# Kernel optimization log

Hardware: AMD Instinct MI355X
Metric: run time of the kernel (lower is better)

The kernel has to match this reference:

```python
import jax, jax.numpy as jnp
import numpy as np

B, C, T = 8, 512, 1024
EXP = 2
E = EXP * C          # 1024, gate/value width
H, HD = 8, 64        # heads, qk head dim
QK = H * HD          # 512
AVG_LEN = 512
EPS = 1e-5


def setup_inputs() -> dict:
    key = jax.random.key(0)
    ks = jax.random.split(key, 10)
    s = 0.02
    return {
        "x": jax.random.normal(ks[0], (B, C, T), jnp.float32),
        "W_in": jax.random.normal(ks[1], (2 * E, C), jnp.float32) * s,
        "b_in": jnp.zeros((2 * E,), jnp.float32),
        "W_attn": jax.random.normal(ks[2], (QK, C), jnp.float32) * s,
        "b_attn": jnp.zeros((QK,), jnp.float32),
        "w_q": 1.0 + jax.random.normal(ks[3], (QK,), jnp.float32) * 0.1,
        "b_q": jax.random.normal(ks[4], (QK,), jnp.float32) * 0.1,
        "w_k": 1.0 + jax.random.normal(ks[5], (QK,), jnp.float32) * 0.1,
        "b_k": jax.random.normal(ks[6], (QK,), jnp.float32) * 0.1,
        "W_out": jax.random.normal(ks[7], (C, E), jnp.float32) * s,
        "b_out": jnp.zeros((C,), jnp.float32),
        "gamma": jnp.ones((C,), jnp.float32),
    }


def reference(x, W_in, b_in, W_attn, b_attn, w_q, b_q, w_k, b_k, W_out, b_out, gamma):
    residual = x
    # mlp_in (1x1 conv) + SiLU, then chunk into gate u and value v, each (B,E,T)
    uv = jax.nn.silu(jnp.einsum('oc,bct->bot', W_in, x) + b_in[:, None])
    u, v = uv[:, :E], uv[:, E:]
    # mlp_attn (1x1 conv); no activation (activation_attn unused in forward)
    z = jnp.einsum('oc,bct->bot', W_attn, x) + b_attn[:, None]  # (B,QK,T)
    # depthwise 1x1 conv on cat(z,z) = two independent per-channel affines
    q = z * w_q[:, None] + b_q[:, None]
    k = z * w_k[:, None] + b_k[:, None]
    # split heads: q,k -> (B,H,T,HD); v -> (B,H,T,E//H)
    q = q.reshape(B, H, HD, T).transpose(0, 1, 3, 2)
    k = k.reshape(B, H, HD, T).transpose(0, 1, 3, 2)
    vh = v.reshape(B, H, E // H, T).transpose(0, 1, 3, 2)
    # entropy-invariant scale: (log n / log avg_len) / sqrt(d)
    scale = (np.log(T) / np.log(AVG_LEN)) / np.sqrt(HD)
    scores = jnp.einsum('bhqd,bhkd->bhqk', q, k) * jnp.float32(scale)
    attn = jax.nn.softmax(scores, axis=-1)
    o = jnp.einsum('bhqk,bhke->bhqe', attn, vh)        # (B,H,T,E//H)
    o = o.transpose(0, 1, 3, 2).reshape(B, E, T)       # back to (B,E,T)
    # gate, project out, residual + RMSNorm over channel dim
    out = jnp.einsum('ce,bet->bct', W_out, u * o) + b_out[:, None]
    y = residual + out
    rms = jax.lax.rsqrt(jnp.mean(y * y, axis=1, keepdims=True) + EPS)
    return y * rms * gamma[:, None]
```

## Files before the change

kernel.cpp:

```cpp
#include <hip/hip_runtime.h>

typedef __attribute__((ext_vector_type(8))) short short8;
typedef __attribute__((ext_vector_type(4))) float f32x4;
typedef __attribute__((ext_vector_type(16))) float f32x16;

__device__ __forceinline__ unsigned short f2b(float f) {
  union { float f; unsigned u; } x; x.f = f;
  unsigned r = (x.u + 0x7fffu + ((x.u >> 16) & 1u)) >> 16;
  return (unsigned short)r;
}
__device__ __forceinline__ float b2f(unsigned short b) {
  union { unsigned u; float f; } x; x.u = ((unsigned)b) << 16;
  return x.f;
}
__device__ __forceinline__ unsigned cvtpk(float lo, float hi) {
  unsigned r;
  asm("v_cvt_pk_bf16_f32 %0, %1, %2" : "=v"(r) : "v"(lo), "v"(hi));
  return r;
}
__device__ __forceinline__ void plswap(unsigned& a, unsigned& b) {
  asm volatile("v_permlane32_swap_b32 %0, %1" : "+v"(a), "+v"(b));
}

#define GLDS16(gp, lp)                                                                  \
  __builtin_amdgcn_global_load_lds((const __attribute__((address_space(1))) void*)(gp), \
                                   (__attribute__((address_space(3))) void*)(lp), 16, 0, 0)

__global__ void prep_w_kernel(const float* __restrict__ W_in, const float* __restrict__ W_attn,
                              const float* __restrict__ W_out, unsigned short* __restrict__ Wcat,
                              unsigned short* __restrict__ WoutB) {
  const int n1 = 2048 * 512, n2 = 512 * 512, n3 = 512 * 1024;
  for (int i = blockIdx.x * 256 + threadIdx.x; i < n1 + n2 + n3; i += gridDim.x * 256) {
    if (i < n1) Wcat[i] = f2b(W_in[i]);
    else if (i < n1 + n2) Wcat[i] = f2b(W_attn[i - n1]);
    else WoutB[i - n1 - n2] = f2b(W_out[i - n1 - n2]);
  }
}

__global__ __launch_bounds__(256) void transpose_x_kernel(const float* __restrict__ x,
                                                          unsigned short* __restrict__ xT) {
  __shared__ float tile[32][33];
  const int bid = blockIdx.x;
  const int b = bid & 7;
  const int rem = bid >> 3;
  const int c0 = (rem >> 5) << 5;
  const int t0 = (rem & 31) << 5;
  const int tj = threadIdx.x & 31, ti = threadIdx.x >> 5;
#pragma unroll
  for (int r = 0; r < 32; r += 8)
    tile[ti + r][tj] = x[(((size_t)b << 9) + c0 + ti + r) * 1024 + t0 + tj];
  __syncthreads();
#pragma unroll
  for (int r = 0; r < 32; r += 8)
    xT[(((size_t)b << 10) + t0 + ti + r) * 512 + c0 + tj] = f2b(tile[tj][ti + r]);
}

__device__ __forceinline__ void gemm_stage(const unsigned short* Ag, const unsigned short* Bg,
                                           int lda, int ldb, int k0, unsigned short* lsA,
                                           unsigned short* lsB, int buf, int sr, int sk,
                                           int ldst) {
  const int bb = buf * 8192;
  GLDS16(Ag + (size_t)sr * lda + k0 + sk, (char*)lsA + bb + ldst);
  GLDS16(Ag + (size_t)(sr + 64) * lda + k0 + sk, (char*)lsA + bb + 4096 + ldst);
  GLDS16(Bg + (size_t)sr * ldb + k0 + sk, (char*)lsB + bb + ldst);
  GLDS16(Bg + (size_t)(sr + 64) * ldb + k0 + sk, (char*)lsB + bb + 4096 + ldst);
}

__device__ __forceinline__ void gemm_bt_core(const unsigned short* __restrict__ Ag,
                                             const unsigned short* __restrict__ Bg, int lda,
                                             int ldb, int K, unsigned short* lsA,
                                             unsigned short* lsB, f32x4 acc[4][4]) {
  const int tid = threadIdx.x;
  const int lane = tid & 63;
  const int w = tid >> 6;
  const int wr = w >> 1, wc = w & 1;
  const int sr = tid >> 2;
  const int sk = (tid & 3) << 3;
  const int ldst = (tid >> 6) << 10;

  const int nt = K >> 5;
  gemm_stage(Ag, Bg, lda, ldb, 0, lsA, lsB, 0, sr, sk, ldst);
  for (int t = 0; t < nt; ++t) {
    const int cur = t & 1;
    if (t + 1 < nt) {
      gemm_stage(Ag, Bg, lda, ldb, (t + 1) << 5, lsA, lsB, cur ^ 1, sr, sk, ldst);
      asm volatile("s_waitcnt vmcnt(4)" ::: "memory");
    } else {
      asm volatile("s_waitcnt vmcnt(0)" ::: "memory");
    }
    __builtin_amdgcn_s_barrier();
    short8 af[4], bfr[4];
    const int bb = cur * 8192;
    const int ko = (lane >> 4) << 4;
    const int ra = (wr << 6) + (lane & 15);
    const int rb = (wc << 6) + (lane & 15);
#pragma unroll
    for (int mi = 0; mi < 4; ++mi)
      af[mi] = *(const short8*)((const char*)lsA + bb + ((ra + (mi << 4)) << 6) + ko);
#pragma unroll
    for (int ni = 0; ni < 4; ++ni)
      bfr[ni] = *(const short8*)((const char*)lsB + bb + ((rb + (ni << 4)) << 6) + ko);
#pragma unroll
    for (int mi = 0; mi < 4; ++mi)
#pragma unroll
      for (int ni = 0; ni < 4; ++ni)
        acc[mi][ni] =
            __builtin_amdgcn_mfma_f32_16x16x32_bf16(af[mi], bfr[ni], acc[mi][ni], 0, 0, 0);
    __builtin_amdgcn_s_barrier();
  }
}

__global__ __launch_bounds__(256) void gemm_a_kernel(
    const unsigned short* __restrict__ Wcat, const unsigned short* __restrict__ xT,
    const float* __restrict__ b_in, const float* __restrict__ b_attn,
    const float* __restrict__ w_q, const float* __restrict__ b_q, const float* __restrict__ w_k,
    const float* __restrict__ b_k, unsigned short* __restrict__ u, unsigned short* __restrict__ v,
    unsigned short* __restrict__ qT, unsigned short* __restrict__ kT) {
  __shared__ __align__(16) unsigned short lsA[8192];
  __shared__ __align__(16) unsigned short lsB[8192];
  const int bid = ((blockIdx.x & 7) * 160) + (blockIdx.x >> 3);
  const int b = bid / 160;
  const int rem = bid % 160;
  const int m0 = (rem >> 3) << 7;
  const int n0 = (rem & 7) << 7;
  f32x4 acc[4][4];
  const f32x4 z4 = {0.f, 0.f, 0.f, 0.f};
#pragma unroll
  for (int mi = 0; mi < 4; ++mi)
#pragma unroll
    for (int ni = 0; ni < 4; ++ni) acc[mi][ni] = z4;

  const unsigned short* Ag = Wcat + (size_t)m0 * 512;
  const unsigned short* Bg = xT + ((size_t)b << 19) + ((size_t)n0 << 9);
  gemm_bt_core(Ag, Bg, 512, 512, 512, lsA, lsB, acc);

  const int lane = threadIdx.x & 63;
  const int w = threadIdx.x >> 6;
  const int wr = w >> 1, wc = w & 1;
#pragma unroll
  for (int mi = 0; mi < 4; ++mi) {
    const int row0 = m0 + (wr << 6) + (mi << 4) + ((lane >> 4) << 2);
#pragma unroll
    for (int ni = 0; ni < 4; ++ni) {
      const int col = n0 + (wc << 6) + (ni << 4) + (lane & 15);
      if (row0 < 2048) {
#pragma unroll
        for (int i = 0; i < 4; ++i) {
          const int row = row0 + i;
          const float s = acc[mi][ni][i] + b_in[row];
          const float r = s / (1.f + __expf(-s));
          if (row < 1024)
            u[((((size_t)b << 10) + row) << 10) + col] = f2b(r);
          else
            v[((((size_t)b << 10) + (row - 1024)) << 10) + col] = f2b(r);
        }
      } else {
        const int c0 = row0 - 2048;
        ushort4 qv, kv;
        unsigned short* qp = (unsigned short*)&qv;
        unsigned short* kp = (unsigned short*)&kv;
#pragma unroll
        for (int i = 0; i < 4; ++i) {
          const int c = c0 + i;
          const float z = acc[mi][ni][i] + b_attn[c];
          qp[i] = f2b(z * w_q[c] + b_q[c]);
          kp[i] = f2b(z * w_k[c] + b_k[c]);
        }
        const int h = c0 >> 6, d = c0 & 63;
        const size_t base = ((((size_t)b * 8 + h) << 10) + col) * 64 + d;
        *(ushort4*)(qT + base) = qv;
        *(ushort4*)(kT + base) = kv;
      }
    }
  }
}

__global__ __launch_bounds__(256, 3) void attn_kernel(const unsigned short* __restrict__ qT,
                                                      const unsigned short* __restrict__ kT,
                                                      const unsigned short* __restrict__ v,
                                                      const unsigned short* __restrict__ u,
                                                      unsigned short* __restrict__ uoT) {
  __shared__ __align__(16) unsigned short Kls[2][4096];
  __shared__ __align__(16) unsigned short Vls[2][8192];
  const float SCALE2 = 0.20037430567f;
  const int bx = blockIdx.x;
  const int xcd = bx & 7, idx = bx >> 3;
  const int bh = (xcd << 3) + (idx & 7);
  const int qb = idx >> 3;
  const int b = bh >> 3, h = bh & 7;
  const int tid = threadIdx.x;
  const int lane = tid & 63;
  const int w = tid >> 6;
  const int l5 = lane >> 5;
  const int l31 = lane & 31;
  const int q0 = qb << 7;

  const unsigned short* qh = qT + ((size_t)bh << 16);
  const unsigned short* kh = kT + ((size_t)bh << 16);
  const unsigned short* vh = v + ((((size_t)b << 10) + (h << 7)) << 10);

  short8 qf[4];
#pragma unroll
  for (int ds = 0; ds < 4; ++ds)
    qf[ds] = *(const short8*)(qh + (size_t)(q0 + (w << 5) + l31) * 64 + (ds << 4) + (l5 << 3));

  f32x16 o[4];
#pragma unroll
  for (int eb = 0; eb < 4; ++eb)
#pragma unroll
    for (int i = 0; i < 16; ++i) o[eb][i] = 0.f;
  float lacc = 0.f;

  const int srow = tid >> 3;
  const int scol = (((tid & 7) ^ (srow & 7)) << 3);

#define ATTN_STAGE(buf, kt)                                                           \
  {                                                                                   \
    const int t2 = (kt) << 6;                                                         \
    GLDS16(kh + (size_t)(t2 + srow) * 64 + scol, (char*)Kls[buf] + (w << 10));        \
    GLDS16(kh + (size_t)(t2 + 32 + srow) * 64 + scol,                                 \
           (char*)Kls[buf] + 4096 + (w << 10));                                       \
    GLDS16(vh + ((size_t)srow << 10) + t2 + scol, (char*)Vls[buf] + (w << 10));       \
    GLDS16(vh + ((size_t)(32 + srow) << 10) + t2 + scol,                              \
           (char*)Vls[buf] + 4096 + (w << 10));                                       \
    GLDS16(vh + ((size_t)(64 + srow) << 10) + t2 + scol,                              \
           (char*)Vls[buf] + 8192 + (w << 10));                                       \
    GLDS16(vh + ((size_t)(96 + srow) << 10) + t2 + scol,                              \
           (char*)Vls[buf] + 12288 + (w << 10));                                      \
  }

  ATTN_STAGE(0, 0);
  union U8 { short8 s8; unsigned u4[4]; };
  for (int kt = 0; kt < 16; ++kt) {
    const int cur = kt & 1;
    if (kt < 15) {
      ATTN_STAGE(cur ^ 1, kt + 1);
      asm volatile("s_waitcnt vmcnt(6)" ::: "memory");
    } else {
      asm volatile("s_waitcnt vmcnt(0)" ::: "memory");
    }
    __builtin_amdgcn_s_barrier();

    const char* kb = (const char*)Kls[cur];
    const char* vb = (const char*)Vls[cur];
    U8 pf[4];

    {
      f32x16 s;
#pragma unroll
      for (int i = 0; i < 16; ++i) s[i] = 0.f;
      const int kr = l31;
      __builtin_amdgcn_s_setprio(1);
#pragma unroll
      for (int ds = 0; ds < 4; ++ds) {
        short8 kf = *(const short8*)(kb + (kr << 7) +
                                     (((ds << 5) + (l5 << 4)) ^ ((kr & 7) << 4)));
        s = __builtin_amdgcn_mfma_f32_32x32x16_bf16(kf, qf[ds], s, 0, 0, 0);
      }
      __builtin_amdgcn_s_setprio(0);
      float p[16];
#pragma unroll
      for (int i = 0; i < 16; ++i) {
        p[i] = exp2f(s[i] * SCALE2);
        lacc += p[i];
      }
      unsigned W00 = cvtpk(p[0], p[1]), W01 = cvtpk(p[2], p[3]);
      unsigned W10 = cvtpk(p[4], p[5]), W11 = cvtpk(p[6], p[7]);
      unsigned W20 = cvtpk(p[8], p[9]), W21 = cvtpk(p[10], p[11]);
      unsigned W30 = cvtpk(p[12], p[13]), W31 = cvtpk(p[14], p[15]);
      unsigned a = W10, bq = W00; plswap(a, bq);
      pf[0].u4[0] = bq; pf[0].u4[2] = a;
      unsigned c = W11, d = W01; plswap(c, d);
      pf[0].u4[1] = d; pf[0].u4[3] = c;
      unsigned e = W30, f = W20; plswap(e, f);
      pf[1].u4[0] = f; pf[1].u4[2] = e;
      unsigned g = W31, hh = W21; plswap(g, hh);
      pf[1].u4[1] = hh; pf[1].u4[3] = g;
    }
    {
      f32x16 s;
#pragma unroll
      for (int i = 0; i < 16; ++i) s[i] = 0.f;
      const int kr = 32 + l31;
      __builtin_amdgcn_s_setprio(1);
#pragma unroll
      for (int ds = 0; ds < 4; ++ds) {
        short8 kf = *(const short8*)(kb + (kr << 7) +
                                     (((ds << 5) + (l5 << 4)) ^ ((kr & 7) << 4)));
        s = __builtin_amdgcn_mfma_f32_32x32x16_bf16(kf, qf[ds], s, 0, 0, 0);
      }
      __builtin_amdgcn_s_setprio(0);
      float p[16];
#pragma unroll
      for (int i = 0; i < 16; ++i) {
        p[i] = exp2f(s[i] * SCALE2);
        lacc += p[i];
      }
      unsigned W00 = cvtpk(p[0], p[1]), W01 = cvtpk(p[2], p[3]);
      unsigned W10 = cvtpk(p[4], p[5]), W11 = cvtpk(p[6], p[7]);
      unsigned W20 = cvtpk(p[8], p[9]), W21 = cvtpk(p[10], p[11]);
      unsigned W30 = cvtpk(p[12], p[13]), W31 = cvtpk(p[14], p[15]);
      unsigned a = W10, bq = W00; plswap(a, bq);
      pf[2].u4[0] = bq; pf[2].u4[2] = a;
      unsigned c = W11, d = W01; plswap(c, d);
      pf[2].u4[1] = d; pf[2].u4[3] = c;
      unsigned e = W30, f = W20; plswap(e, f);
      pf[3].u4[0] = f; pf[3].u4[2] = e;
      unsigned g = W31, hh = W21; plswap(g, hh);
      pf[3].u4[1] = hh; pf[3].u4[3] = g;
    }

    __builtin_amdgcn_s_setprio(1);
#pragma unroll
    for (int eb = 0; eb < 4; ++eb) {
      const int vrow = (eb << 5) + l31;
#pragma unroll
      for (int ks = 0; ks < 4; ++ks) {
        short8 vf = *(const short8*)(vb + (vrow << 7) +
                                     (((ks << 5) + (l5 << 4)) ^ ((vrow & 7) << 4)));
        o[eb] = __builtin_amdgcn_mfma_f32_32x32x16_bf16(vf, pf[ks].s8, o[eb], 0, 0, 0);
      }
    }
    __builtin_amdgcn_s_setprio(0);
    __builtin_amdgcn_s_barrier();
  }
#undef ATTN_STAGE

  lacc += __shfl_xor(lacc, 32, 64);
  const float rl = 1.f / lacc;
  const int t = q0 + (w << 5) + l31;

#pragma unroll
  for (int eb = 0; eb < 4; ++eb) {
#pragma unroll
    for (int g = 0; g < 4; ++g) {
      const int e4 = (eb << 5) + (g << 3) + (l5 << 2);
      const int eg = (h << 7) + e4;
      ushort4 outv;
      unsigned short* op = (unsigned short*)&outv;
#pragma unroll
      for (int j = 0; j < 4; ++j) {
        const int i = (g << 2) + j;
        const float oo = o[eb][i] * rl;
        const float uu = b2f(u[((((size_t)b << 10) + eg + j) << 10) + t]);
        op[j] = f2b(oo * uu);
      }
      *(ushort4*)(uoT + ((((size_t)b << 10) + t) << 10) + eg) = outv;
    }
  }
}

__global__ __launch_bounds__(256) void gemm_c_kernel(const unsigned short* __restrict__ uoT,
                                                     const unsigned short* __restrict__ WoutB,
                                                     const float* __restrict__ x,
                                                     const float* __restrict__ b_out,
                                                     unsigned short* __restrict__ y) {
  __shared__ __align__(16) unsigned short lsA[8192];
  __shared__ __align__(16) unsigned short lsB[8192];
  const int bid = ((blockIdx.x & 7) * 32) + (blockIdx.x >> 3);
  const int b = bid >> 5;
  const int rem = bid & 31;
  const int m0 = (rem >> 2) << 7;
  const int n0 = (rem & 3) << 7;
  f32x4 acc[4][4];
  const f32x4 z4 = {0.f, 0.f, 0.f, 0.f};
#pragma unroll
  for (int mi = 0; mi < 4; ++mi)
#pragma unroll
    for (int ni = 0; ni < 4; ++ni) acc[mi][ni] = z4;

  const unsigned short* Ag = uoT + ((size_t)b << 20) + ((size_t)m0 << 10);
  const unsigned short* Bg = WoutB + ((size_t)n0 << 10);
  gemm_bt_core(Ag, Bg, 1024, 1024, 1024, lsA, lsB, acc);

  const int lane = threadIdx.x & 63;
  const int w = threadIdx.x >> 6;
  const int wr = w >> 1, wc = w & 1;
#pragma unroll
  for (int mi = 0; mi < 4; ++mi) {
    const int t4 = m0 + (wr << 6) + (mi << 4) + ((lane >> 4) << 2);
#pragma unroll
    for (int ni = 0; ni < 4; ++ni) {
      const int c = n0 + (wc << 6) + (ni << 4) + (lane & 15);
      const size_t base = ((((size_t)b << 9) + c) << 10) + t4;
      const f32x4 xv = *(const f32x4*)(x + base);
      const float bo = b_out[c];
      ushort4 ov;
      unsigned short* op = (unsigned short*)&ov;
#pragma unroll
      for (int i = 0; i < 4; ++i) op[i] = f2b(acc[mi][ni][i] + bo + xv[i]);
      *(ushort4*)(y + base) = ov;
    }
  }
}

__global__ __launch_bounds__(256) void rms_kernel(const unsigned short* __restrict__ y,
                                                  const float* __restrict__ gamma,
                                                  float* __restrict__ out) {
  __shared__ float part[8][32];
  __shared__ float rmsv[32];
  const int bid = blockIdx.x;
  const int b = bid >> 5;
  const int t0 = (bid & 31) << 5;
  const int tid = threadIdx.x;
  const int tt = tid & 31, cg = tid >> 5;
  const int t = t0 + tt;
  float vals[64];
  float ss = 0.f;
#pragma unroll
  for (int ci = 0; ci < 64; ++ci) {
    const int c = (cg << 6) + ci;
    const float vv = b2f(y[((((size_t)b << 9) + c) << 10) + t]);
    vals[ci] = vv;
    ss += vv * vv;
  }
  part[cg][tt] = ss;
  __syncthreads();
  if (tid < 32) {
    float tot = 0.f;
#pragma unroll
    for (int g = 0; g < 8; ++g) tot += part[g][tid];
    rmsv[tid] = rsqrtf(tot / 512.f + 1e-5f);
  }
  __syncthreads();
  const float rm = rmsv[tt];
#pragma unroll
  for (int ci = 0; ci < 64; ++ci) {
    const int c = (cg << 6) + ci;
    out[((((size_t)b << 9) + c) << 10) + t] = vals[ci] * rm * gamma[c];
  }
}

extern "C" void kernel_launch(void* const* d_in, const int* in_sizes, int n_in, void* d_out,
                              int out_size, void* d_ws, size_t ws_size, hipStream_t stream) {
  const float* x = (const float*)d_in[0];
  const float* W_in = (const float*)d_in[1];
  const float* b_in = (const float*)d_in[2];
  const float* W_attn = (const float*)d_in[3];
  const float* b_attn = (const float*)d_in[4];
  const float* w_q = (const float*)d_in[5];
  const float* b_q = (const float*)d_in[6];
  const float* w_k = (const float*)d_in[7];
  const float* b_k = (const float*)d_in[8];
  const float* W_out = (const float*)d_in[9];
  const float* b_out = (const float*)d_in[10];
  const float* gamma = (const float*)d_in[11];
  float* out = (float*)d_out;

  char* ws = (char*)d_ws;
  size_t off = 0;
  auto alloc = [&](size_t bytes) {
    char* p = ws + off;
    off += (bytes + 255) & ~(size_t)255;
    return p;
  };
  unsigned short* Wcat = (unsigned short*)alloc((size_t)2560 * 512 * 2);
  unsigned short* WoutB = (unsigned short*)alloc((size_t)512 * 1024 * 2);
  unsigned short* xT = (unsigned short*)alloc((size_t)8 * 1024 * 512 * 2);
  unsigned short* u = (unsigned short*)alloc((size_t)8 * 1024 * 1024 * 2);
  unsigned short* v = (unsigned short*)alloc((size_t)8 * 1024 * 1024 * 2);
  unsigned short* qT = (unsigned short*)alloc((size_t)8 * 8 * 1024 * 64 * 2);
  unsigned short* kT = (unsigned short*)alloc((size_t)8 * 8 * 1024 * 64 * 2);
  unsigned short* uoT = (unsigned short*)alloc((size_t)8 * 1024 * 1024 * 2);
  unsigned short* y = (unsigned short*)alloc((size_t)8 * 512 * 1024 * 2);
  if (off > ws_size) return;

  prep_w_kernel<<<896, 256, 0, stream>>>(W_in, W_attn, W_out, Wcat, WoutB);
  transpose_x_kernel<<<4096, 256, 0, stream>>>(x, xT);
  gemm_a_kernel<<<1280, 256, 0, stream>>>(Wcat, xT, b_in, b_attn, w_q, b_q, w_k, b_k, u, v, qT,
                                          kT);
  attn_kernel<<<512, 256, 0, stream>>>(qT, kT, v, u, uoT);
  gemm_c_kernel<<<256, 256, 0, stream>>>(uoT, WoutB, x, b_out, y);
  rms_kernel<<<256, 256, 0, stream>>>(y, gamma, out);
}
```

Before: 129.4 us.

## Triple-buffer LDS staging in GEMM and attention kernels, drop trailing barrier

Switches the GEMM core and the attention K/V staging from double to triple buffering in LDS. Loads are issued two tiles ahead, after the single per-iteration barrier, and buffer indices rotate, so the second barrier at the end of each iteration can be removed. This aims to hide more global-load latency and cut synchronization. In exchange it uses more LDS per block, and the attention kernel's launch bound drops from 3 to 2 blocks per CU, which may reduce occupancy.

Measured after the change: 124.6 us. 3.7% less time.

```diff
diff --git a/kernel.cpp b/kernel.cpp
--- a/kernel.cpp
+++ b/kernel.cpp
@@ -79,18 +79,20 @@
   const int ldst = (tid >> 6) << 10;
 
   const int nt = K >> 5;
+  int c0b = 0, c1b = 1, c2b = 2;
   gemm_stage(Ag, Bg, lda, ldb, 0, lsA, lsB, 0, sr, sk, ldst);
+  gemm_stage(Ag, Bg, lda, ldb, 32, lsA, lsB, 1, sr, sk, ldst);
   for (int t = 0; t < nt; ++t) {
-    const int cur = t & 1;
     if (t + 1 < nt) {
-      gemm_stage(Ag, Bg, lda, ldb, (t + 1) << 5, lsA, lsB, cur ^ 1, sr, sk, ldst);
       asm volatile("s_waitcnt vmcnt(4)" ::: "memory");
     } else {
       asm volatile("s_waitcnt vmcnt(0)" ::: "memory");
     }
     __builtin_amdgcn_s_barrier();
+    if (t + 2 < nt)
+      gemm_stage(Ag, Bg, lda, ldb, (t + 2) << 5, lsA, lsB, c2b, sr, sk, ldst);
     short8 af[4], bfr[4];
-    const int bb = cur * 8192;
+    const int bb = c0b * 8192;
     const int ko = (lane >> 4) << 4;
     const int ra = (wr << 6) + (lane & 15);
     const int rb = (wc << 6) + (lane & 15);
@@ -106,7 +108,7 @@
       for (int ni = 0; ni < 4; ++ni)
         acc[mi][ni] =
             __builtin_amdgcn_mfma_f32_16x16x32_bf16(af[mi], bfr[ni], acc[mi][ni], 0, 0, 0);
-    __builtin_amdgcn_s_barrier();
+    const int tmp = c0b; c0b = c1b; c1b = c2b; c2b = tmp;
   }
 }
 
@@ -116,8 +118,8 @@
     const float* __restrict__ w_q, const float* __restrict__ b_q, const float* __restrict__ w_k,
     const float* __restrict__ b_k, unsigned short* __restrict__ u, unsigned short* __restrict__ v,
     unsigned short* __restrict__ qT, unsigned short* __restrict__ kT) {
-  __shared__ __align__(16) unsigned short lsA[8192];
-  __shared__ __align__(16) unsigned short lsB[8192];
+  __shared__ __align__(16) unsigned short lsA[12288];
+  __shared__ __align__(16) unsigned short lsB[12288];
   const int bid = ((blockIdx.x & 7) * 160) + (blockIdx.x >> 3);
   const int b = bid / 160;
   const int rem = bid % 160;
@@ -175,13 +177,13 @@
   }
 }
 
-__global__ __launch_bounds__(256, 3) void attn_kernel(const unsigned short* __restrict__ qT,
+__global__ __launch_bounds__(256, 2) void attn_kernel(const unsigned short* __restrict__ qT,
                                                       const unsigned short* __restrict__ kT,
                                                       const unsigned short* __restrict__ v,
                                                       const unsigned short* __restrict__ u,
                                                       unsigned short* __restrict__ uoT) {
-  __shared__ __align__(16) unsigned short Kls[2][4096];
-  __shared__ __align__(16) unsigned short Vls[2][8192];
+  __shared__ __align__(16) unsigned short Kls[3 * 4096];
+  __shared__ __align__(16) unsigned short Vls[3 * 8192];
   const float SCALE2 = 0.20037430567f;
   const int bx = blockIdx.x;
   const int xcd = bx & 7, idx = bx >> 3;
@@ -214,35 +216,34 @@
   const int srow = tid >> 3;
   const int scol = (((tid & 7) ^ (srow & 7)) << 3);
 
-#define ATTN_STAGE(buf, kt)                                                           \
-  {                                                                                   \
-    const int t2 = (kt) << 6;                                                         \
-    GLDS16(kh + (size_t)(t2 + srow) * 64 + scol, (char*)Kls[buf] + (w << 10));        \
-    GLDS16(kh + (size_t)(t2 + 32 + srow) * 64 + scol,                                 \
-           (char*)Kls[buf] + 4096 + (w << 10));                                       \
-    GLDS16(vh + ((size_t)srow << 10) + t2 + scol, (char*)Vls[buf] + (w << 10));       \
-    GLDS16(vh + ((size_t)(32 + srow) << 10) + t2 + scol,                              \
-           (char*)Vls[buf] + 4096 + (w << 10));                                       \
-    GLDS16(vh + ((size_t)(64 + srow) << 10) + t2 + scol,                              \
-           (char*)Vls[buf] + 8192 + (w << 10));                                       \
-    GLDS16(vh + ((size_t)(96 + srow) << 10) + t2 + scol,                              \
-           (char*)Vls[buf] + 12288 + (w << 10));                                      \
-  }
-
+#define ATTN_STAGE(buf, kt)                                                            \
+  {                                                                                    \
+    const int t2 = (kt) << 6;                                                          \
+    char* kbase = (char*)Kls + (buf)*8192;                                             \
+    char* vbase = (char*)Vls + (buf)*16384;                                            \
+    GLDS16(kh + (size_t)(t2 + srow) * 64 + scol, kbase + (w << 10));                   \
+    GLDS16(kh + (size_t)(t2 + 32 + srow) * 64 + scol, kbase + 4096 + (w << 10));       \
+    GLDS16(vh + ((size_t)srow << 10) + t2 + scol, vbase + (w << 10));                  \
+    GLDS16(vh + ((size_t)(32 + srow) << 10) + t2 + scol, vbase + 4096 + (w << 10));    \
+    GLDS16(vh + ((size_t)(64 + srow) << 10) + t2 + scol, vbase + 8192 + (w << 10));    \
+    GLDS16(vh + ((size_t)(96 + srow) << 10) + t2 + scol, vbase + 12288 + (w << 10));   \
+  }
+
+  int c0b = 0, c1b = 1, c2b = 2;
   ATTN_STAGE(0, 0);
+  ATTN_STAGE(1, 1);
   union U8 { short8 s8; unsigned u4[4]; };
   for (int kt = 0; kt < 16; ++kt) {
-    const int cur = kt & 1;
     if (kt < 15) {
-      ATTN_STAGE(cur ^ 1, kt + 1);
       asm volatile("s_waitcnt vmcnt(6)" ::: "memory");
     } else {
       asm volatile("s_waitcnt vmcnt(0)" ::: "memory");
     }
     __builtin_amdgcn_s_barrier();
-
-    const char* kb = (const char*)Kls[cur];
-    const char* vb = (const char*)Vls[cur];
+    if (kt < 14) ATTN_STAGE(c2b, kt + 2);
+
+    const char* kb = (const char*)Kls + c0b * 8192;
+    const char* vb = (const char*)Vls + c0b * 16384;
     U8 pf[4];
 
     {
@@ -322,7 +323,7 @@
       }
     }
     __builtin_amdgcn_s_setprio(0);
-    __builtin_amdgcn_s_barrier();
+    const int tmp = c0b; c0b = c1b; c1b = c2b; c2b = tmp;
   }
 #undef ATTN_STAGE
 
@@ -355,8 +356,8 @@
                                                      const float* __restrict__ x,
                                                      const float* __restrict__ b_out,
                                                      unsigned short* __restrict__ y) {
-  __shared__ __align__(16) unsigned short lsA[8192];
-  __shared__ __align__(16) unsigned short lsB[8192];
+  __shared__ __align__(16) unsigned short lsA[12288];
+  __shared__ __align__(16) unsigned short lsB[12288];
   const int bid = ((blockIdx.x & 7) * 32) + (blockIdx.x >> 3);
   const int b = bid >> 5;
   const int rem = bid & 31;
```
